# Kernel optimization log

Measured on AMD Instinct MI355X. Metric: run time of the kernel, lower is better.

## Reference

```python
import jax, jax.numpy as jnp
import numpy as np
from jax import lax

N_EMBD = 1024
N_HEAD = 16
HEAD_DIM = N_EMBD // N_HEAD
EPS = 1e-6
B, T = 4, 2048


def setup_inputs() -> dict:
    key = jax.random.key(0)
    ks = jax.random.split(key, 5)
    scale = 1.0 / np.sqrt(N_EMBD)
    return {
        "x": jax.random.normal(ks[0], (B, T, N_EMBD), jnp.float32),
        "W_attn": jax.random.normal(ks[1], (N_EMBD, 3 * N_EMBD), jnp.float32) * scale,
        "b_attn": jax.random.normal(ks[2], (3 * N_EMBD,), jnp.float32) * 0.01,
        "W_proj": jax.random.normal(ks[3], (N_EMBD, N_EMBD), jnp.float32) * scale,
        "b_proj": jax.random.normal(ks[4], (N_EMBD,), jnp.float32) * 0.01,
    }


def _feature_map(x):
    # ELU + 1 for non-negativity
    return jax.nn.elu(x) + 1.0


def reference(x, W_attn, b_attn, W_proj, b_proj):
    Bb, Tt, C = x.shape
    qkv = x @ W_attn + b_attn  # (B,T,3C)
    q, k, v = jnp.split(qkv, 3, axis=-1)

    def to_heads(t):
        # (B,T,C) -> (T,B,H,d): scan axis leading
        return t.reshape(Bb, Tt, N_HEAD, HEAD_DIM).transpose(1, 0, 2, 3)

    q = _feature_map(to_heads(q))
    k = _feature_map(to_heads(k))
    v = to_heads(v)

    # Causal linear attention: O(d^2) running state instead of the torch
    # code's materialized (B,H,T,d,d) cumsum — same math.
    def step(carry, inp):
        kv, ksum = carry  # (B,H,d,d), (B,H,d)
        qt, kt, vt = inp  # each (B,H,d)
        kv = kv + kt[..., :, None] * vt[..., None, :]
        ksum = ksum + kt
        num = jnp.einsum('bhi,bhij->bhj', qt, kv)
        den = jnp.einsum('bhi,bhi->bh', qt, ksum)[..., None] + EPS
        return (kv, ksum), num / den

    init = (
        jnp.zeros((Bb, N_HEAD, HEAD_DIM, HEAD_DIM), x.dtype),
        jnp.zeros((Bb, N_HEAD, HEAD_DIM), x.dtype),
    )
    _, y = lax.scan(step, init, (q, k, v))  # (T,B,H,d)
    y = y.transpose(1, 0, 2, 3).reshape(Bb, Tt, C)
    return y @ W_proj + b_proj  # dropout is identity in eval mode
```

## Files before the change

kernel.cpp:

```cpp
#include <hip/hip_runtime.h>
#include <math.h>

#define BB   4
#define TT   2048
#define CC   1024
#define HH   16
#define DD   64
#define MM   (BB*TT)
#define NQKV (3*CC)
#define LCH  128
#define NCH  (TT/LCH)
#define EPSF 1e-6f

#define QKST 72
#define PST  136
#define VTST 136

typedef __bf16 bf16x8 __attribute__((ext_vector_type(8)));
typedef float  floatx4 __attribute__((ext_vector_type(4)));

__device__ __forceinline__ unsigned short f2bf(float f) {
  union { float f; unsigned int u; } v; v.f = f;
  unsigned int r = v.u + 0x7fffu + ((v.u >> 16) & 1u);
  return (unsigned short)(r >> 16);
}
__device__ __forceinline__ float bf2f(unsigned short s) {
  union { unsigned int u; float f; } v; v.u = ((unsigned int)s) << 16;
  return v.f;
}
__device__ __forceinline__ float featmap(float v) {
  return v > 0.f ? v + 1.f : __expf(v);
}
__device__ __forceinline__ void gld_lds_b128(const unsigned short* g, unsigned short* l) {
  __builtin_amdgcn_global_load_lds(
      (const __attribute__((address_space(1))) unsigned int*)g,
      (__attribute__((address_space(3))) unsigned int*)l, 16, 0, 0);
}


__global__ __launch_bounds__(256) void cvt_x_kernel(const float* __restrict__ x,
                                                    unsigned short* __restrict__ xb, int n) {
  int i = (blockIdx.x * 256 + threadIdx.x) * 4;
  if (i < n) {
    float4 f = *(const float4*)(x + i);
    ushort4 o;
    o.x = f2bf(f.x); o.y = f2bf(f.y); o.z = f2bf(f.z); o.w = f2bf(f.w);
    *(ushort4*)(xb + i) = o;
  }
}

__global__ __launch_bounds__(256) void transpose_cvt_kernel(const float* __restrict__ W,
                                                            unsigned short* __restrict__ out,
                                                            int R, int Cc) {
  __shared__ float tile[32][33];
  int bx = blockIdx.x * 32;
  int by = blockIdx.y * 32;
  int tx = threadIdx.x, ty = threadIdx.y;
  #pragma unroll
  for (int i = ty; i < 32; i += 8)
    tile[i][tx] = W[(size_t)(by + i) * Cc + bx + tx];
  __syncthreads();
  #pragma unroll
  for (int i = ty; i < 32; i += 8)
    out[(size_t)(bx + i) * R + by + tx] = f2bf(tile[tx][i]);
}

#define GEMM_K_LOOP(A_, Bt_, K_)                                                 \
  __shared__ __align__(16) unsigned short As[128 * 32];                          \
  __shared__ __align__(16) unsigned short Bs[128 * 32];                          \
  int tid = threadIdx.x;                                                         \
  int wave = tid >> 6, lane = tid & 63;                                          \
  int lr = lane & 15, lq = lane >> 4;                                            \
  int m0 = blockIdx.y * 128, n0 = blockIdx.x * 128;                              \
  int wm = (wave >> 1) * 64, wn = (wave & 1) * 64;                               \
  int lrow = lane >> 2;                      \
  int lk = (lane & 3) ^ (lrow & 3);                 \
  int ci0 = wave * 2;                                                            \
  const unsigned short* gA0 = A_ + (size_t)(m0 + ci0 * 16 + lrow) * K_ + lk * 8; \
  const unsigned short* gA1 = gA0 + 16 * K_;                                     \
  const unsigned short* gB0 = Bt_ + (size_t)(n0 + ci0 * 16 + lrow) * K_ + lk * 8;\
  const unsigned short* gB1 = gB0 + 16 * K_;                                     \
  unsigned short* lA0 = As + ci0 * 512;                                          \
  unsigned short* lB0 = Bs + ci0 * 512;                                          \
  floatx4 acc[4][4] = {};                                                        \
  for (int k0 = 0; k0 < K_; k0 += 32) {                                          \
    __syncthreads();                 \
    gld_lds_b128(gA0 + k0, lA0);                                                 \
    gld_lds_b128(gA1 + k0, lA0 + 512);                                           \
    gld_lds_b128(gB0 + k0, lB0);                                                 \
    gld_lds_b128(gB1 + k0, lB0 + 512);                                           \
    __syncthreads();                                    \
    bf16x8 af[4], bfr[4];                                                        \
    _Pragma("unroll")                                                            \
    for (int i = 0; i < 4; i++)                                                  \
      af[i] = *(const bf16x8*)&As[(wm + i * 16 + lr) * 32 + ((lq ^ (lr & 3)) << 3)]; \
    _Pragma("unroll")                                                            \
    for (int j = 0; j < 4; j++)                                                  \
      bfr[j] = *(const bf16x8*)&Bs[(wn + j * 16 + lr) * 32 + ((lq ^ (lr & 3)) << 3)]; \
    _Pragma("unroll")                                                            \
    for (int i = 0; i < 4; i++)                                                  \
      _Pragma("unroll")                                                          \
      for (int j = 0; j < 4; j++)                                                \
        acc[i][j] = __builtin_amdgcn_mfma_f32_16x16x32_bf16(af[i], bfr[j], acc[i][j], 0, 0, 0); \
  }

__global__ __launch_bounds__(256) void gemm_qkv_kernel(
    const unsigned short* __restrict__ A, const unsigned short* __restrict__ Bt,
    const float* __restrict__ bias,
    unsigned short* __restrict__ qh, unsigned short* __restrict__ kh,
    unsigned short* __restrict__ vh) {
  GEMM_K_LOOP(A, Bt, CC)
  #pragma unroll
  for (int i = 0; i < 4; i++) {
    #pragma unroll
    for (int j = 0; j < 4; j++) {
      #pragma unroll
      for (int r = 0; r < 4; r++) {
        int row = wm + i * 16 + lq * 4 + r;
        int col = wn + j * 16 + lr;
        int m = m0 + row, n = n0 + col;
        float v = acc[i][j][r] + bias[n];
        int which = n >> 10, c = n & 1023;
        int h = c >> 6, dd = c & 63;
        int b = m >> 11, t = m & 2047;
        size_t idx = (((size_t)(b * HH + h)) * TT + t) * DD + dd;
        if (which == 0)      qh[idx] = f2bf(featmap(v));
        else if (which == 1) kh[idx] = f2bf(featmap(v));
        else                 vh[idx] = f2bf(v);
      }
    }
  }
}

__global__ __launch_bounds__(256) void gemm_proj_kernel(
    const unsigned short* __restrict__ A, const unsigned short* __restrict__ Bt,
    const float* __restrict__ bias, float* __restrict__ out) {
  GEMM_K_LOOP(A, Bt, CC)
  #pragma unroll
  for (int i = 0; i < 4; i++) {
    #pragma unroll
    for (int j = 0; j < 4; j++) {
      #pragma unroll
      for (int r = 0; r < 4; r++) {
        int row = wm + i * 16 + lq * 4 + r;
        int col = wn + j * 16 + lr;
        int m = m0 + row, n = n0 + col;
        out[(size_t)m * CC + n] = acc[i][j][r] + bias[n];
      }
    }
  }
}

__global__ __launch_bounds__(256) void chunk_state_kernel(
    const unsigned short* __restrict__ kh, const unsigned short* __restrict__ vh,
    float* __restrict__ KV, float* __restrict__ Ksum) {
  int blk = blockIdx.x;
  int bh = blk / NCH, c = blk % NCH;
  const unsigned short* kp = kh + ((size_t)bh * TT + c * LCH) * DD;
  const unsigned short* vp = vh + ((size_t)bh * TT + c * LCH) * DD;
  __shared__ float ks[LCH * DD];
  __shared__ float vs[LCH * DD];
  for (int e = threadIdx.x; e < LCH * DD; e += 256) {
    ks[e] = bf2f(kp[e]);
    vs[e] = bf2f(vp[e]);
  }
  __syncthreads();
  int j = threadIdx.x & 63, i0 = (threadIdx.x >> 6) * 16;
  float acc[16];
  #pragma unroll
  for (int ii = 0; ii < 16; ii++) acc[ii] = 0.f;
  for (int t = 0; t < LCH; t++) {
    float vv = vs[t * DD + j];
    #pragma unroll
    for (int ii = 0; ii < 16; ii++) acc[ii] += ks[t * DD + i0 + ii] * vv;
  }
  float* kvout = KV + (size_t)blk * DD * DD;
  #pragma unroll
  for (int ii = 0; ii < 16; ii++) kvout[(i0 + ii) * DD + j] = acc[ii];
  if (threadIdx.x < DD) {
    int i = threadIdx.x;
    float s = 0.f;
    for (int t = 0; t < LCH; t++) s += ks[t * DD + i];
    Ksum[(size_t)blk * DD + i] = s;
  }
}

__global__ __launch_bounds__(256) void prefix_state_kernel(const float* __restrict__ KV,
                                                           const float* __restrict__ Ksum,
                                                           unsigned short* __restrict__ SPb) {
  int bh = blockIdx.x;
  int tid = threadIdx.x;
  int i = tid >> 2;
  int j0 = (tid & 3) * 16;
  float run[16];
  #pragma unroll
  for (int ii = 0; ii < 16; ii++) run[ii] = 0.f;
  float krun = 0.f;
  for (int c = 0; c < NCH; c++) {
    size_t base = ((size_t)bh * NCH + c) * (80 * 64);
    const float* kv = KV + ((size_t)bh * NCH + c) * (DD * DD) + (size_t)i * DD + j0;
    #pragma unroll
    for (int jj = 0; jj < 16; jj++) {
      SPb[base + (size_t)(j0 + jj) * 64 + i] = f2bf(run[jj]);
      run[jj] += kv[jj];
    }
    if (tid < DD) {
      SPb[base + 64 * 64 + tid] = f2bf(krun);
      krun += Ksum[((size_t)bh * NCH + c) * DD + tid];
    }
    for (int e = tid; e < 15 * 64; e += 256)
      SPb[base + 65 * 64 + e] = 0;
  }
}

__global__ __launch_bounds__(256) void chunk_attn_kernel(
    const unsigned short* __restrict__ qh, const unsigned short* __restrict__ kh,
    const unsigned short* __restrict__ vh, const unsigned short* __restrict__ SPb,
    unsigned short* __restrict__ yb) {
  __shared__ __align__(16) unsigned short lds[128 * QKST * 2 + 80 * VTST];
  unsigned short* Qs = lds;
  unsigned short* Ks = lds + 128 * QKST;
  unsigned short* P  = lds;
  unsigned short* Vt = lds + 128 * QKST * 2;

  int blk = blockIdx.x;
  int bh = blk / NCH, c = blk % NCH;
  int b = bh / HH, h = bh % HH;
  int tid = threadIdx.x;
  const unsigned short* qp = qh + ((size_t)bh * TT + c * LCH) * DD;
  const unsigned short* kp = kh + ((size_t)bh * TT + c * LCH) * DD;
  const unsigned short* vp = vh + ((size_t)bh * TT + c * LCH) * DD;

  for (int e = tid; e < 1024; e += 256) {
    int row = e >> 3, k8 = (e & 7) * 8;
    *(uint4*)&Qs[row * QKST + k8] = *(const uint4*)&qp[(size_t)row * DD + k8];
    *(uint4*)&Ks[row * QKST + k8] = *(const uint4*)&kp[(size_t)row * DD + k8];
  }
  {
    int t = tid & 127;
    for (int j8 = (tid >> 7) * 8; j8 < DD; j8 += 16) {
      union { uint4 u; unsigned short s[8]; } w;
      w.u = *(const uint4*)&vp[(size_t)t * DD + j8];
      #pragma unroll
      for (int jj = 0; jj < 8; jj++) Vt[(j8 + jj) * VTST + t] = w.s[jj];
    }
  }
  for (int e = tid; e < 16 * 128; e += 256) {
    int rr = e >> 7, n = e & 127;
    Vt[(64 + rr) * VTST + n] = (rr == 0) ? (unsigned short)0x3F80 : (unsigned short)0;
  }
  __syncthreads();

  int wave = tid >> 6, lane = tid & 63;
  int lr = lane & 15, lq = lane >> 4;
  int mbase = wave * 32;

  bf16x8 aq[2][2];
  #pragma unroll
  for (int i = 0; i < 2; i++)
    #pragma unroll
    for (int kk = 0; kk < 2; kk++)
      aq[i][kk] = *(const bf16x8*)&Qs[(mbase + i * 16 + lr) * QKST + kk * 32 + lq * 8];

  floatx4 acc[2][5] = {};
  const unsigned short* spb = SPb + (size_t)blk * (80 * 64);
  #pragma unroll
  for (int jt = 0; jt < 5; jt++)
    #pragma unroll
    for (int kk = 0; kk < 2; kk++) {
      bf16x8 bsp = *(const bf16x8*)&spb[(jt * 16 + lr) * 64 + kk * 32 + lq * 8];
      acc[0][jt] = __builtin_amdgcn_mfma_f32_16x16x32_bf16(aq[0][kk], bsp, acc[0][jt], 0, 0, 0);
      acc[1][jt] = __builtin_amdgcn_mfma_f32_16x16x32_bf16(aq[1][kk], bsp, acc[1][jt], 0, 0, 0);
    }
  floatx4 sacc[2][8] = {};
  #pragma unroll
  for (int nt = 0; nt < 8; nt++)
    #pragma unroll
    for (int kk = 0; kk < 2; kk++) {
      bf16x8 bk = *(const bf16x8*)&Ks[(nt * 16 + lr) * QKST + kk * 32 + lq * 8];
      sacc[0][nt] = __builtin_amdgcn_mfma_f32_16x16x32_bf16(aq[0][kk], bk, sacc[0][nt], 0, 0, 0);
      sacc[1][nt] = __builtin_amdgcn_mfma_f32_16x16x32_bf16(aq[1][kk], bk, sacc[1][nt], 0, 0, 0);
    }
  __syncthreads();

  #pragma unroll
  for (int i = 0; i < 2; i++)
    #pragma unroll
    for (int nt = 0; nt < 8; nt++) {
      int col = nt * 16 + lr;
      #pragma unroll
      for (int r = 0; r < 4; r++) {
        int m = mbase + i * 16 + lq * 4 + r;
        float v = (col <= m) ? sacc[i][nt][r] : 0.f;
        P[m * PST + col] = f2bf(v);
      }
    }
  __syncthreads();

  #pragma unroll
  for (int kk4 = 0; kk4 < 4; kk4++) {
    bf16x8 ap0 = *(const bf16x8*)&P[(mbase + lr) * PST + kk4 * 32 + lq * 8];
    bf16x8 ap1 = *(const bf16x8*)&P[(mbase + 16 + lr) * PST + kk4 * 32 + lq * 8];
    #pragma unroll
    for (int jt = 0; jt < 5; jt++) {
      bf16x8 bv = *(const bf16x8*)&Vt[(jt * 16 + lr) * VTST + kk4 * 32 + lq * 8];
      acc[0][jt] = __builtin_amdgcn_mfma_f32_16x16x32_bf16(ap0, bv, acc[0][jt], 0, 0, 0);
      acc[1][jt] = __builtin_amdgcn_mfma_f32_16x16x32_bf16(ap1, bv, acc[1][jt], 0, 0, 0);
    }
  }

  int srclane = lq << 4;
  #pragma unroll
  for (int i = 0; i < 2; i++) {
    #pragma unroll
    for (int r = 0; r < 4; r++) {
      float den = __shfl(acc[i][4][r], srclane, 64);
      float inv = 1.f / (den + EPSF);
      int tg = c * LCH + mbase + i * 16 + lq * 4 + r;
      size_t base = ((size_t)b * TT + tg) * CC + h * DD;
      #pragma unroll
      for (int jt = 0; jt < 4; jt++)
        yb[base + jt * 16 + lr] = f2bf(acc[i][jt][r] * inv);
    }
  }
}

extern "C" void kernel_launch(void* const* d_in, const int* in_sizes, int n_in,
                              void* d_out, int out_size, void* d_ws, size_t ws_size,
                              hipStream_t stream) {
  const float* x      = (const float*)d_in[0];
  const float* W_attn = (const float*)d_in[1];
  const float* b_attn = (const float*)d_in[2];
  const float* W_proj = (const float*)d_in[3];
  const float* b_proj = (const float*)d_in[4];
  float* out = (float*)d_out;

  char* ws = (char*)d_ws;
  size_t off = 0;
  auto alloc = [&](size_t bytes) -> char* {
    char* p = ws + off;
    off += (bytes + 255) & ~(size_t)255;
    return p;
  };
  unsigned short* xb  = (unsigned short*)alloc((size_t)MM * CC * 2);
  unsigned short* WaT = (unsigned short*)alloc((size_t)NQKV * CC * 2);
  unsigned short* WpT = (unsigned short*)alloc((size_t)CC * CC * 2);
  unsigned short* qh  = (unsigned short*)alloc((size_t)MM * CC * 2);
  unsigned short* kh  = (unsigned short*)alloc((size_t)MM * CC * 2);
  unsigned short* vh  = (unsigned short*)alloc((size_t)MM * CC * 2);
  float* KV   = (float*)alloc((size_t)BB * HH * NCH * DD * DD * 4);
  float* Ksum = (float*)alloc((size_t)BB * HH * NCH * DD * 4);
  unsigned short* SPb = (unsigned short*)alloc((size_t)BB * HH * NCH * 80 * 64 * 2);
  unsigned short* yb = xb;

  cvt_x_kernel<<<(MM * CC) / 1024, 256, 0, stream>>>(x, xb, MM * CC);
  transpose_cvt_kernel<<<dim3(NQKV / 32, CC / 32), dim3(32, 8), 0, stream>>>(W_attn, WaT, CC, NQKV);
  transpose_cvt_kernel<<<dim3(CC / 32, CC / 32), dim3(32, 8), 0, stream>>>(W_proj, WpT, CC, CC);
  gemm_qkv_kernel<<<dim3(NQKV / 128, MM / 128), 256, 0, stream>>>(xb, WaT, b_attn, qh, kh, vh);
  chunk_state_kernel<<<BB * HH * NCH, 256, 0, stream>>>(kh, vh, KV, Ksum);
  prefix_state_kernel<<<BB * HH, 256, 0, stream>>>(KV, Ksum, SPb);
  chunk_attn_kernel<<<BB * HH * NCH, 256, 0, stream>>>(qh, kh, vh, SPb, yb);
  gemm_proj_kernel<<<dim3(CC / 128, MM / 128), 256, 0, stream>>>(yb, WpT, b_proj, out);
}
```

Baseline: 264.7 us.

## Use MFMA for chunk state, widen GEMM K-tile, parallelize prefix scan

The GEMM K-loop now stages 64-wide K tiles with an 8-way XOR swizzle, which halves the number of barrier pairs per tile. The per-chunk K^T V state is computed with bf16 MFMA on transposed LDS tiles instead of fp32 scalar FMAs. A ones row is appended to V so that Ksum falls out of the same matmul, and the result is written directly in the padded 80x64 transposed layout. The prefix scan is spread across 5x more blocks using vectorized float4 loads and coalesced stores. The trade-offs are lower precision in the state accumulation inputs (bf16) and doubled LDS use in the GEMM.

```diff
diff --git a/kernel.cpp b/kernel.cpp
--- a/kernel.cpp
+++ b/kernel.cpp
@@ -66,42 +66,44 @@
 }
 
 #define GEMM_K_LOOP(A_, Bt_, K_)                                                 \
-  __shared__ __align__(16) unsigned short As[128 * 32];                          \
-  __shared__ __align__(16) unsigned short Bs[128 * 32];                          \
+  __shared__ __align__(16) unsigned short As[128 * 64];                          \
+  __shared__ __align__(16) unsigned short Bs[128 * 64];                          \
   int tid = threadIdx.x;                                                         \
   int wave = tid >> 6, lane = tid & 63;                                          \
   int lr = lane & 15, lq = lane >> 4;                                            \
   int m0 = blockIdx.y * 128, n0 = blockIdx.x * 128;                              \
   int wm = (wave >> 1) * 64, wn = (wave & 1) * 64;                               \
-  int lrow = lane >> 2;                      \
-  int lk = (lane & 3) ^ (lrow & 3);                 \
-  int ci0 = wave * 2;                                                            \
-  const unsigned short* gA0 = A_ + (size_t)(m0 + ci0 * 16 + lrow) * K_ + lk * 8; \
-  const unsigned short* gA1 = gA0 + 16 * K_;                                     \
-  const unsigned short* gB0 = Bt_ + (size_t)(n0 + ci0 * 16 + lrow) * K_ + lk * 8;\
-  const unsigned short* gB1 = gB0 + 16 * K_;                                     \
-  unsigned short* lA0 = As + ci0 * 512;                                          \
-  unsigned short* lB0 = Bs + ci0 * 512;                                          \
+  int lrow = lane >> 3;                        \
+  int lk = (lane & 7) ^ lrow;                       \
+  int rbase = wave * 32;                                                         \
+  const unsigned short* gA = A_ + (size_t)(m0 + rbase + lrow) * K_ + lk * 8;     \
+  const unsigned short* gB = Bt_ + (size_t)(n0 + rbase + lrow) * K_ + lk * 8;    \
+  unsigned short* lA = As + rbase * 64;                                          \
+  unsigned short* lB = Bs + rbase * 64;                                          \
   floatx4 acc[4][4] = {};                                                        \
-  for (int k0 = 0; k0 < K_; k0 += 32) {                                          \
+  for (int k0 = 0; k0 < K_; k0 += 64) {                                          \
     __syncthreads();                 \
-    gld_lds_b128(gA0 + k0, lA0);                                                 \
-    gld_lds_b128(gA1 + k0, lA0 + 512);                                           \
-    gld_lds_b128(gB0 + k0, lB0);                                                 \
-    gld_lds_b128(gB1 + k0, lB0 + 512);                                           \
+    _Pragma("unroll")                                                            \
+    for (int g = 0; g < 4; g++) {                                                \
+      gld_lds_b128(gA + k0 + (size_t)g * 8 * K_, lA + g * 512);                  \
+      gld_lds_b128(gB + k0 + (size_t)g * 8 * K_, lB + g * 512);                  \
+    }                                                                            \
     __syncthreads();                                    \
-    bf16x8 af[4], bfr[4];                                                        \
     _Pragma("unroll")                                                            \
-    for (int i = 0; i < 4; i++)                                                  \
-      af[i] = *(const bf16x8*)&As[(wm + i * 16 + lr) * 32 + ((lq ^ (lr & 3)) << 3)]; \
-    _Pragma("unroll")                                                            \
-    for (int j = 0; j < 4; j++)                                                  \
-      bfr[j] = *(const bf16x8*)&Bs[(wn + j * 16 + lr) * 32 + ((lq ^ (lr & 3)) << 3)]; \
-    _Pragma("unroll")                                                            \
-    for (int i = 0; i < 4; i++)                                                  \
+    for (int kk = 0; kk < 2; kk++) {                                             \
+      bf16x8 af[4], bfr[4];                                                      \
+      _Pragma("unroll")                                                          \
+      for (int i = 0; i < 4; i++)                                                \
+        af[i] = *(const bf16x8*)&As[(wm + i * 16 + lr) * 64 + ((((kk << 2) + lq) ^ (lr & 7)) << 3)]; \
       _Pragma("unroll")                                                          \
       for (int j = 0; j < 4; j++)                                                \
-        acc[i][j] = __builtin_amdgcn_mfma_f32_16x16x32_bf16(af[i], bfr[j], acc[i][j], 0, 0, 0); \
+        bfr[j] = *(const bf16x8*)&Bs[(wn + j * 16 + lr) * 64 + ((((kk << 2) + lq) ^ (lr & 7)) << 3)]; \
+      _Pragma("unroll")                                                          \
+      for (int i = 0; i < 4; i++)                                                \
+        _Pragma("unroll")                                                        \
+        for (int j = 0; j < 4; j++)                                              \
+          acc[i][j] = __builtin_amdgcn_mfma_f32_16x16x32_bf16(af[i], bfr[j], acc[i][j], 0, 0, 0); \
+    }                                                                            \
   }
 
 __global__ __launch_bounds__(256) void gemm_qkv_kernel(
@@ -153,63 +155,65 @@
 
 __global__ __launch_bounds__(256) void chunk_state_kernel(
     const unsigned short* __restrict__ kh, const unsigned short* __restrict__ vh,
-    float* __restrict__ KV, float* __restrict__ Ksum) {
+    float* __restrict__ KVx) {
+  __shared__ __align__(16) unsigned short Kt[64 * VTST];
+  __shared__ __align__(16) unsigned short Vt[80 * VTST];
   int blk = blockIdx.x;
   int bh = blk / NCH, c = blk % NCH;
+  int tid = threadIdx.x;
   const unsigned short* kp = kh + ((size_t)bh * TT + c * LCH) * DD;
   const unsigned short* vp = vh + ((size_t)bh * TT + c * LCH) * DD;
-  __shared__ float ks[LCH * DD];
-  __shared__ float vs[LCH * DD];
-  for (int e = threadIdx.x; e < LCH * DD; e += 256) {
-    ks[e] = bf2f(kp[e]);
-    vs[e] = bf2f(vp[e]);
-  }
-  __syncthreads();
-  int j = threadIdx.x & 63, i0 = (threadIdx.x >> 6) * 16;
-  float acc[16];
-  #pragma unroll
-  for (int ii = 0; ii < 16; ii++) acc[ii] = 0.f;
-  for (int t = 0; t < LCH; t++) {
-    float vv = vs[t * DD + j];
-    #pragma unroll
-    for (int ii = 0; ii < 16; ii++) acc[ii] += ks[t * DD + i0 + ii] * vv;
-  }
-  float* kvout = KV + (size_t)blk * DD * DD;
-  #pragma unroll
-  for (int ii = 0; ii < 16; ii++) kvout[(i0 + ii) * DD + j] = acc[ii];
-  if (threadIdx.x < DD) {
-    int i = threadIdx.x;
-    float s = 0.f;
-    for (int t = 0; t < LCH; t++) s += ks[t * DD + i];
-    Ksum[(size_t)blk * DD + i] = s;
-  }
-}
-
-__global__ __launch_bounds__(256) void prefix_state_kernel(const float* __restrict__ KV,
-                                                           const float* __restrict__ Ksum,
+  {
+    int t = tid & 127;
+    for (int j8 = (tid >> 7) * 8; j8 < DD; j8 += 16) {
+      union { uint4 u; unsigned short s[8]; } wk, wv;
+      wk.u = *(const uint4*)&kp[(size_t)t * DD + j8];
+      wv.u = *(const uint4*)&vp[(size_t)t * DD + j8];
+      #pragma unroll
+      for (int jj = 0; jj < 8; jj++) {
+        Kt[(j8 + jj) * VTST + t] = wk.s[jj];
+        Vt[(j8 + jj) * VTST + t] = wv.s[jj];
+      }
+    }
+  }
+  for (int e = tid; e < 16 * 128; e += 256) {
+    int rr = e >> 7, n = e & 127;
+    Vt[(64 + rr) * VTST + n] = (rr == 0) ? (unsigned short)0x3F80 : (unsigned short)0;
+  }
+  __syncthreads();
+  int wave = tid >> 6, lane = tid & 63;
+  int lr = lane & 15, lq = lane >> 4;
+  int i0 = wave * 16;
+  floatx4 acc[5] = {};
+  #pragma unroll
+  for (int kk = 0; kk < 4; kk++) {
+    bf16x8 a = *(const bf16x8*)&Kt[(i0 + lr) * VTST + kk * 32 + lq * 8];
+    #pragma unroll
+    for (int jt = 0; jt < 5; jt++) {
+      bf16x8 b = *(const bf16x8*)&Vt[(jt * 16 + lr) * VTST + kk * 32 + lq * 8];
+      acc[jt] = __builtin_amdgcn_mfma_f32_16x16x32_bf16(a, b, acc[jt], 0, 0, 0);
+    }
+  }
+  float* o = KVx + (size_t)blk * 5120;
+  #pragma unroll
+  for (int jt = 0; jt < 5; jt++)
+    #pragma unroll
+    for (int r = 0; r < 4; r++)
+      o[(jt * 16 + lr) * 64 + i0 + lq * 4 + r] = acc[jt][r];
+}
+
+__global__ __launch_bounds__(256) void prefix_state_kernel(const float* __restrict__ KVx,
                                                            unsigned short* __restrict__ SPb) {
-  int bh = blockIdx.x;
-  int tid = threadIdx.x;
-  int i = tid >> 2;
-  int j0 = (tid & 3) * 16;
-  float run[16];
-  #pragma unroll
-  for (int ii = 0; ii < 16; ii++) run[ii] = 0.f;
-  float krun = 0.f;
+  int bh = blockIdx.x / 5, jb = blockIdx.x % 5;
+  int e = jb * 1024 + threadIdx.x * 4;
+  float run0 = 0.f, run1 = 0.f, run2 = 0.f, run3 = 0.f;
   for (int c = 0; c < NCH; c++) {
-    size_t base = ((size_t)bh * NCH + c) * (80 * 64);
-    const float* kv = KV + ((size_t)bh * NCH + c) * (DD * DD) + (size_t)i * DD + j0;
-    #pragma unroll
-    for (int jj = 0; jj < 16; jj++) {
-      SPb[base + (size_t)(j0 + jj) * 64 + i] = f2bf(run[jj]);
-      run[jj] += kv[jj];
-    }
-    if (tid < DD) {
-      SPb[base + 64 * 64 + tid] = f2bf(krun);
-      krun += Ksum[((size_t)bh * NCH + c) * DD + tid];
-    }
-    for (int e = tid; e < 15 * 64; e += 256)
-      SPb[base + 65 * 64 + e] = 0;
+    size_t base = ((size_t)bh * NCH + c) * 5120 + e;
+    float4 v = *(const float4*)&KVx[base];
+    ushort4 o;
+    o.x = f2bf(run0); o.y = f2bf(run1); o.z = f2bf(run2); o.w = f2bf(run3);
+    *(ushort4*)&SPb[base] = o;
+    run0 += v.x; run1 += v.y; run2 += v.z; run3 += v.w;
   }
 }
 
@@ -348,8 +352,7 @@
   unsigned short* qh  = (unsigned short*)alloc((size_t)MM * CC * 2);
   unsigned short* kh  = (unsigned short*)alloc((size_t)MM * CC * 2);
   unsigned short* vh  = (unsigned short*)alloc((size_t)MM * CC * 2);
-  float* KV   = (float*)alloc((size_t)BB * HH * NCH * DD * DD * 4);
-  float* Ksum = (float*)alloc((size_t)BB * HH * NCH * DD * 4);
+  float* KVx = (float*)alloc((size_t)BB * HH * NCH * 80 * 64 * 4);
   unsigned short* SPb = (unsigned short*)alloc((size_t)BB * HH * NCH * 80 * 64 * 2);
   unsigned short* yb = xb;
 
@@ -357,8 +360,8 @@
   transpose_cvt_kernel<<<dim3(NQKV / 32, CC / 32), dim3(32, 8), 0, stream>>>(W_attn, WaT, CC, NQKV);
   transpose_cvt_kernel<<<dim3(CC / 32, CC / 32), dim3(32, 8), 0, stream>>>(W_proj, WpT, CC, CC);
   gemm_qkv_kernel<<<dim3(NQKV / 128, MM / 128), 256, 0, stream>>>(xb, WaT, b_attn, qh, kh, vh);
-  chunk_state_kernel<<<BB * HH * NCH, 256, 0, stream>>>(kh, vh, KV, Ksum);
-  prefix_state_kernel<<<BB * HH, 256, 0, stream>>>(KV, Ksum, SPb);
+  chunk_state_kernel<<<BB * HH * NCH, 256, 0, stream>>>(kh, vh, KVx);
+  prefix_state_kernel<<<BB * HH * 5, 256, 0, stream>>>(KVx, SPb);
   chunk_attn_kernel<<<BB * HH * NCH, 256, 0, stream>>>(qh, kh, vh, SPb, yb);
   gemm_proj_kernel<<<dim3(CC / 128, MM / 128), 256, 0, stream>>>(yb, WpT, b_proj, out);
 }
```

New measurement: 244.6 us. 7.6% less time.
